# Kernel optimization log

Hardware: AMD Instinct MI355X
Metric: run time of the kernel (lower is better)

Reference implementation:

```python
import jax, jax.numpy as jnp
import numpy as np

ALPHA = 1.0
SPLIT = 4


def setup_inputs() -> dict:
    key = jax.random.key(0)
    k1, k2 = jax.random.split(key)
    prediction = jax.random.normal(k1, (8, 19, 512, 512), dtype=jnp.float32)
    weights = jax.random.uniform(k2, (SPLIT * SPLIT, SPLIT * SPLIT), dtype=jnp.float32)
    return {"prediction": prediction, "weights": weights}


def reference(prediction, weights):
    S = SPLIT
    B, C, H, W = prediction.shape
    # resample(): h = int((H/S)/10), then bilinear resize to (h*S, w*S),
    # align_corners=False == half-pixel centers == jax.image.resize 'bilinear'.
    h = (H // S) // 10
    w = (W // S) // 10
    x = jax.image.resize(prediction, (B, C, h * S, w * S), method="bilinear")
    # Split into S*S patches of size [B,C,h,w] and flatten each patch.
    # The original nested loops over shifts (i,j) and patches (n,m) compute
    # map_input[n*S+m, ((n+i)%S)*S+((m+j)%S)] = mean((patch[(n+i)%S,(m+j)%S] - patch[n,m])^2),
    # which over all shifts is exactly the full pairwise mean-squared-difference matrix.
    P = x.reshape(B, C, S, h, S, w).transpose(2, 4, 0, 1, 3, 5).reshape(S * S, -1)
    diff = P[None, :, :] - P[:, None, :]          # [S^2, S^2, B*C*h*w] (~22 MB)
    map_input = jnp.mean(diff * diff, axis=-1)    # [S^2, S^2]
    value = (map_input * weights).mean()
    return value * ALPHA
```

## Files before the change

kernel.cpp:

```cpp
#include <hip/hip_runtime.h>


#define HIN 512
#define WOUT 48
#define NTAP 22
#define NBC 152
#define NPAIR 24
#define NBLK (NBC * NPAIR)
#define TSTRIDE 580
#define GROUP 12
#define KS (512.0 / 48.0)

struct WTab {
  float hw[NTAP][WOUT];
  int hst[WOUT];
  constexpr WTab() : hw{}, hst{} {
    for (int i = 0; i < WOUT; ++i) {
      double s = (i + 0.5) * KS - 0.5;
      double v = s - KS;
      long long tt = (long long)v;
      int stc = (int)((v > (double)tt) ? tt + 1 : tt);
      if (stc < 0) stc = 0;
      if (stc > HIN - NTAP) stc = HIN - NTAP;
      double wr[NTAP] = {};
      double sum = 0.0;
      for (int k = 0; k < NTAP; ++k) {
        int j = stc + k;
        double d = s - (double)j;
        if (d < 0) d = -d;
        double wv = 1.0 - d * (1.0 / KS);
        if (wv < 0.0) wv = 0.0;
        if (j >= HIN) wv = 0.0;
        wr[k] = wv;
        sum += wv;
      }
      for (int k = 0; k < NTAP; ++k) hw[k][i] = (float)(wr[k] / sum);
      hst[i] = stc;
    }
  }
};
__constant__ WTab WT{};

__global__ __launch_bounds__(256, 6) void k_resize(const float* __restrict__ pred,
                                                   float* __restrict__ smallimg,
                                                   float* __restrict__ out) {
  __shared__ float tile[2][TSTRIDE];

  const int t = threadIdx.x;
  const int wid = (blockIdx.x & 7) * (NBLK / 8) + (blockIdx.x >> 3);
  const int bc = wid / NPAIR;
  const int pair = wid - bc * NPAIR;

  if (blockIdx.x == 0 && t == 0) out[0] = 0.f;

  const int slot = t >> 7;
  const int oy = pair * 2 + slot;
  const int x = (t & 127) << 2;
  const int base = WT.hst[oy];
  const float* p = pred + (size_t)bc * (HIN * HIN) + (size_t)base * HIN + x;
  float4 a = make_float4(0.f, 0.f, 0.f, 0.f);
#pragma unroll
  for (int k = 0; k < NTAP; ++k) {
    const float4 v = *reinterpret_cast<const float4*>(p + (size_t)k * HIN);
    const float wk = WT.hw[k][oy];
    a.x = fmaf(wk, v.x, a.x);
    a.y = fmaf(wk, v.y, a.y);
    a.z = fmaf(wk, v.z, a.z);
    a.w = fmaf(wk, v.w, a.w);
  }
  *reinterpret_cast<float4*>(&tile[slot][x + ((x >> 5) << 2)]) = a;
  __syncthreads();

  if (t < 2 * WOUT) {
    const int r = (t >= WOUT) ? 1 : 0;
    const int j = t - r * WOUT;
    const int stc = WT.hst[j];
    float acc = 0.f;
#pragma unroll
    for (int k = 0; k < NTAP; ++k) {
      const int cc = stc + k;
      acc = fmaf(WT.hw[k][j], tile[r][cc + ((cc >> 5) << 2)], acc);
    }
    smallimg[(size_t)bc * (WOUT * WOUT) + (pair * 2 + r) * WOUT + j] = acc;
  }
}

__global__ __launch_bounds__(256) void k_gram(const float* __restrict__ smallimg,
                                              const float* __restrict__ wts,
                                              float* __restrict__ out) {
  __shared__ float img[WOUT * WOUT];
  __shared__ float Gs[256];
  __shared__ float partial[4];

  const int tid = threadIdx.x;
  const float* src = smallimg + (size_t)blockIdx.x * (WOUT * WOUT);
  for (int idx = tid; idx < (WOUT * WOUT) / 4; idx += 256) {
    *reinterpret_cast<float4*>(&img[idx * 4]) =
        *reinterpret_cast<const float4*>(src + idx * 4);
  }
  __syncthreads();
  const int a = tid >> 4;
  const int b = tid & 15;
  const float* pa = &img[((a >> 2) * GROUP) * WOUT + (a & 3) * GROUP];
  const float* pb = &img[((b >> 2) * GROUP) * WOUT + (b & 3) * GROUP];
  float acc = 0.f;
  for (int y = 0; y < GROUP; ++y) {
#pragma unroll
    for (int q = 0; q < 3; ++q) {
      const float4 va = *reinterpret_cast<const float4*>(pa + y * WOUT + q * 4);
      const float4 vb = *reinterpret_cast<const float4*>(pb + y * WOUT + q * 4);
      acc += va.x * vb.x + va.y * vb.y + va.z * vb.z + va.w * vb.w;
    }
  }
  Gs[tid] = acc;
  __syncthreads();

  float v = wts[tid] * (Gs[a * 17] + Gs[b * 17] - 2.0f * Gs[tid]);
#pragma unroll
  for (int off = 32; off > 0; off >>= 1) v += __shfl_down(v, off, 64);
  if ((tid & 63) == 0) partial[tid >> 6] = v;
  __syncthreads();
  if (tid == 0) {
    atomicAdd(out, (partial[0] + partial[1] + partial[2] + partial[3]) *
                       (float)(1.0 / (256.0 * 21888.0)));
  }
}

extern "C" void kernel_launch(void* const* d_in, const int* in_sizes, int n_in,
                              void* d_out, int out_size, void* d_ws, size_t ws_size,
                              hipStream_t stream) {
  const float* pred = (const float*)d_in[0];
  const float* wts = (const float*)d_in[1];
  float* out = (float*)d_out;
  float* smallimg = (float*)((char*)d_ws + 2048);

  hipLaunchKernelGGL(k_resize, dim3(NBLK), dim3(256), 0, stream, pred, smallimg, out);
  hipLaunchKernelGGL(k_gram, dim3(NBC), dim3(256), 0, stream, smallimg, wts, out);
}
```

Before: 34.89 us.

## Fuse resize and Gram reduction into one kernel with per-row partial Grams

Merges the resize and Gram kernels into one kernel. Each 512-thread block computes the four resized rows that share a within-patch row index, one per patch row. From those it builds a partial 16x16 Gram and adds its weighted contribution straight to the output. This removes the intermediate small-image round trip through global memory and the second kernel launch. In exchange, the output is zeroed with a separate memset, and many more blocks issue atomic adds to the same scalar.

```diff
diff --git a/kernel.cpp b/kernel.cpp
--- a/kernel.cpp
+++ b/kernel.cpp
@@ -5,10 +5,8 @@
 #define WOUT 48
 #define NTAP 22
 #define NBC 152
-#define NPAIR 24
-#define NBLK (NBC * NPAIR)
+#define NBLK (NBC * 12)
 #define TSTRIDE 580
-#define GROUP 12
 #define KS (512.0 / 48.0)
 
 struct WTab {
@@ -41,38 +39,39 @@
 };
 __constant__ WTab WT{};
 
-__global__ __launch_bounds__(256, 6) void k_resize(const float* __restrict__ pred,
-                                                   float* __restrict__ smallimg,
-                                                   float* __restrict__ out) {
-  __shared__ float tile[2][TSTRIDE];
+__global__ __launch_bounds__(512, 4) void k_fused(const float* __restrict__ pred,
+                                                  const float* __restrict__ wts,
+                                                  float* __restrict__ out) {
+  __shared__ float tile[4][TSTRIDE];
+  __shared__ float img4[4][WOUT];
+  __shared__ float Gs[256];
+  __shared__ float partial[4];
 
   const int t = threadIdx.x;
   const int wid = (blockIdx.x & 7) * (NBLK / 8) + (blockIdx.x >> 3);
-  const int bc = wid / NPAIR;
-  const int pair = wid - bc * NPAIR;
+  const int bc = wid / 12;
+  const int y = wid - bc * 12;
 
-  if (blockIdx.x == 0 && t == 0) out[0] = 0.f;
-
-  const int slot = t >> 7;
-  const int oy = pair * 2 + slot;
+  const int s = t >> 7;
+  const int oy = s * 12 + y;
   const int x = (t & 127) << 2;
   const int base = WT.hst[oy];
   const float* p = pred + (size_t)bc * (HIN * HIN) + (size_t)base * HIN + x;
-  float4 a = make_float4(0.f, 0.f, 0.f, 0.f);
+  float4 a4 = make_float4(0.f, 0.f, 0.f, 0.f);
 #pragma unroll
   for (int k = 0; k < NTAP; ++k) {
     const float4 v = *reinterpret_cast<const float4*>(p + (size_t)k * HIN);
     const float wk = WT.hw[k][oy];
-    a.x = fmaf(wk, v.x, a.x);
-    a.y = fmaf(wk, v.y, a.y);
-    a.z = fmaf(wk, v.z, a.z);
-    a.w = fmaf(wk, v.w, a.w);
+    a4.x = fmaf(wk, v.x, a4.x);
+    a4.y = fmaf(wk, v.y, a4.y);
+    a4.z = fmaf(wk, v.z, a4.z);
+    a4.w = fmaf(wk, v.w, a4.w);
   }
-  *reinterpret_cast<float4*>(&tile[slot][x + ((x >> 5) << 2)]) = a;
+  *reinterpret_cast<float4*>(&tile[s][x + ((x >> 5) << 2)]) = a4;
   __syncthreads();
 
-  if (t < 2 * WOUT) {
-    const int r = (t >= WOUT) ? 1 : 0;
+  if (t < 4 * WOUT) {
+    const int r = t / WOUT;
     const int j = t - r * WOUT;
     const int stc = WT.hst[j];
     float acc = 0.f;
@@ -81,46 +80,33 @@
       const int cc = stc + k;
       acc = fmaf(WT.hw[k][j], tile[r][cc + ((cc >> 5) << 2)], acc);
     }
-    smallimg[(size_t)bc * (WOUT * WOUT) + (pair * 2 + r) * WOUT + j] = acc;
-  }
-}
-
-__global__ __launch_bounds__(256) void k_gram(const float* __restrict__ smallimg,
-                                              const float* __restrict__ wts,
-                                              float* __restrict__ out) {
-  __shared__ float img[WOUT * WOUT];
-  __shared__ float Gs[256];
-  __shared__ float partial[4];
-
-  const int tid = threadIdx.x;
-  const float* src = smallimg + (size_t)blockIdx.x * (WOUT * WOUT);
-  for (int idx = tid; idx < (WOUT * WOUT) / 4; idx += 256) {
-    *reinterpret_cast<float4*>(&img[idx * 4]) =
-        *reinterpret_cast<const float4*>(src + idx * 4);
+    img4[r][j] = acc;
   }
   __syncthreads();
-  const int a = tid >> 4;
-  const int b = tid & 15;
-  const float* pa = &img[((a >> 2) * GROUP) * WOUT + (a & 3) * GROUP];
-  const float* pb = &img[((b >> 2) * GROUP) * WOUT + (b & 3) * GROUP];
-  float acc = 0.f;
-  for (int y = 0; y < GROUP; ++y) {
+
+  const int a = t >> 4;
+  const int b = t & 15;
+  if (t < 256) {
+    const float* pa = &img4[a >> 2][(a & 3) * 12];
+    const float* pb = &img4[b >> 2][(b & 3) * 12];
+    float acc = 0.f;
 #pragma unroll
     for (int q = 0; q < 3; ++q) {
-      const float4 va = *reinterpret_cast<const float4*>(pa + y * WOUT + q * 4);
-      const float4 vb = *reinterpret_cast<const float4*>(pb + y * WOUT + q * 4);
+      const float4 va = *reinterpret_cast<const float4*>(pa + q * 4);
+      const float4 vb = *reinterpret_cast<const float4*>(pb + q * 4);
       acc += va.x * vb.x + va.y * vb.y + va.z * vb.z + va.w * vb.w;
     }
+    Gs[t] = acc;
   }
-  Gs[tid] = acc;
   __syncthreads();
 
-  float v = wts[tid] * (Gs[a * 17] + Gs[b * 17] - 2.0f * Gs[tid]);
+  float v = 0.f;
+  if (t < 256) v = wts[t] * (Gs[a * 17] + Gs[b * 17] - 2.0f * Gs[t]);
 #pragma unroll
   for (int off = 32; off > 0; off >>= 1) v += __shfl_down(v, off, 64);
-  if ((tid & 63) == 0) partial[tid >> 6] = v;
+  if (t < 256 && (t & 63) == 0) partial[t >> 6] = v;
   __syncthreads();
-  if (tid == 0) {
+  if (t == 0) {
     atomicAdd(out, (partial[0] + partial[1] + partial[2] + partial[3]) *
                        (float)(1.0 / (256.0 * 21888.0)));
   }
@@ -132,8 +118,7 @@
   const float* pred = (const float*)d_in[0];
   const float* wts = (const float*)d_in[1];
   float* out = (float*)d_out;
-  float* smallimg = (float*)((char*)d_ws + 2048);
 
-  hipLaunchKernelGGL(k_resize, dim3(NBLK), dim3(256), 0, stream, pred, smallimg, out);
-  hipLaunchKernelGGL(k_gram, dim3(NBC), dim3(256), 0, stream, smallimg, wts, out);
+  hipMemsetAsync(out, 0, sizeof(float), stream);
+  hipLaunchKernelGGL(k_fused, dim3(NBLK), dim3(512), 0, stream, pred, wts, out);
 }
```

Result: slower. 45.08 us (+29.2%).
